# Kernel optimization log

Hardware: AMD Instinct MI355X
Metric: run time of the kernel (lower is better)

Reference implementation:

```python
import jax, jax.numpy as jnp
import numpy as np


def setup_inputs() -> dict:
    key = jax.random.key(0)
    inputs = jax.random.normal(key, (64, 4096, 256), dtype=jnp.float32)
    return {"inputs": inputs}


def reference(inputs) -> jnp.ndarray:
    # inputs: [B, N, D]; tfp.stats.covariance(sample_axis=1) -> population cov [B, D, D]
    B, N, D = inputs.shape
    mean = jnp.mean(inputs, axis=1, keepdims=True)            # [B, 1, D]
    xc = inputs - mean                                        # centered samples
    cov = jnp.einsum('bnd,bne->bde', xc, xc) / N              # [B, D, D]
    # band_part(ones, 0, -1) keeps the UPPER triangle (incl. diagonal);
    # boolean_mask flattens row-major -> triu entries in row-major order.
    iu, ju = jnp.triu_indices(D)
    return cov[:, iu, ju]                                     # [B, D*(D+1)//2]
```

## Files before the change

### kernel.cpp

```cpp
#include <hip/hip_runtime.h>
#include <hip/hip_bf16.h>
#include <stdint.h>

typedef unsigned short u16;
typedef unsigned int   u32;

#define NB   64
#define NN   4096
#define ND   256
#define NTRI 32896
#define NSPLIT 4
#define KROWS  1024
#define NCHUNK 16

__device__ __forceinline__ u32 cvtpk(float lo, float hi) {
  u32 r;
  asm("v_cvt_pk_bf16_f32 %0, %1, %2" : "=v"(r) : "v"(lo), "v"(hi));
  return r;
}
__device__ __forceinline__ float b2f_lo(u32 v) {
  union { u32 u; float f; } x; x.u = v << 16; return x.f;
}
__device__ __forceinline__ float b2f_hi(u32 v) {
  union { u32 u; float f; } x; x.u = v & 0xffff0000u; return x.f;
}

typedef __attribute__((ext_vector_type(8))) __bf16 bf16x8;
typedef __attribute__((ext_vector_type(4))) float  f32x4;

__global__ __launch_bounds__(768) void k_cov(const float* __restrict__ in,
                                             u16* __restrict__ covp,
                                             float* __restrict__ part) {
  __shared__ alignas(16) u16 Lt[2][2][256][32];
  __shared__ float msum[8][256];

  int blk = blockIdx.x;
  int b = blk >> 2, s = blk & 3;
  int t = threadIdx.x;
  int w = t >> 6, lane = t & 63;

  int tsel = w >> 2;
  int quad = w & 3;
  int wr = quad >> 1, wc = quad & 1;
  int ti = (tsel == 2) ? 1 : 0;
  int tj = (tsel == 0) ? 0 : 1;
  bool diag = (ti == tj);
  bool alive = !(diag && quad == 2);
  int fr = lane & 15, fg = lane >> 4;
  int dpA = ti * 128 + wr * 64;
  int dpB = tj * 128 + wc * 64;

  int aoffB[4], boffB[4];
  int jj = (fg ^ (fr >> 2)) << 4;
#pragma unroll
  for (int m = 0; m < 4; ++m) aoffB[m] = (dpA + m * 16 + fr) * 64 + jj;
#pragma unroll
  for (int n = 0; n < 4; ++n) boffB[n] = (dpB + n * 16 + fr) * 64 + jj;

  bool stager = (w < 8);
  int c4 = lane;
  int ksw = w >> 2;
  int xw = w & 3;
  int swz = ((xw ^ (c4 & 3)) << 4);

  f32x4 acc[4][4];
  f32x4 zero = {0.f, 0.f, 0.f, 0.f};
#pragma unroll
  for (int m = 0; m < 4; ++m)
#pragma unroll
    for (int n = 0; n < 4; ++n) acc[m][n] = zero;

  const float4* in4 = (const float4*)(in + (size_t)b * NN * ND);
  int rbase0 = (s * KROWS + w * 8) * 64 + c4;

  float4 ms = make_float4(0.f, 0.f, 0.f, 0.f);
  float4 s0, s1, s2, s3, s4, s5, s6, s7;
  uint4 q0, q1, q2, q3;

#define ISSUE(C)                                                \
  if (stager && (C) < NCHUNK) {                                 \
    int rb = rbase0 + (C) * 4096;                               \
    s0 = in4[rb + 0 * 64]; s1 = in4[rb + 1 * 64];               \
    s2 = in4[rb + 2 * 64]; s3 = in4[rb + 3 * 64];               \
    s4 = in4[rb + 4 * 64]; s5 = in4[rb + 5 * 64];               \
    s6 = in4[rb + 6 * 64]; s7 = in4[rb + 7 * 64];               \
  }

#define CVT()                                                                 \
  if (stager) {                                                               \
    ms.x += s0.x + s1.x + s2.x + s3.x + s4.x + s5.x + s6.x + s7.x;            \
    ms.y += s0.y + s1.y + s2.y + s3.y + s4.y + s5.y + s6.y + s7.y;            \
    ms.z += s0.z + s1.z + s2.z + s3.z + s4.z + s5.z + s6.z + s7.z;            \
    ms.w += s0.w + s1.w + s2.w + s3.w + s4.w + s5.w + s6.w + s7.w;            \
    q0 = make_uint4(cvtpk(s0.x, s1.x), cvtpk(s2.x, s3.x),                     \
                    cvtpk(s4.x, s5.x), cvtpk(s6.x, s7.x));                    \
    q1 = make_uint4(cvtpk(s0.y, s1.y), cvtpk(s2.y, s3.y),                     \
                    cvtpk(s4.y, s5.y), cvtpk(s6.y, s7.y));                    \
    q2 = make_uint4(cvtpk(s0.z, s1.z), cvtpk(s2.z, s3.z),                     \
                    cvtpk(s4.z, s5.z), cvtpk(s6.z, s7.z));                    \
    q3 = make_uint4(cvtpk(s0.w, s1.w), cvtpk(s2.w, s3.w),                     \
                    cvtpk(s4.w, s5.w), cvtpk(s6.w, s7.w));                    \
  }

#define WRITE(BUF)                                                            \
  if (stager) {                                                               \
    char* pl = (char*)&Lt[BUF][ksw][0][0] + swz;                              \
    *(uint4*)(pl + (c4 * 4 + 0) * 64) = q0;                                   \
    *(uint4*)(pl + (c4 * 4 + 1) * 64) = q1;                                   \
    *(uint4*)(pl + (c4 * 4 + 2) * 64) = q2;                                   \
    *(uint4*)(pl + (c4 * 4 + 3) * 64) = q3;                                   \
  }

#define COMPUTE(BUF)                                                          \
  if (alive) {                                                                \
    _Pragma("unroll")                                                         \
    for (int ks = 0; ks < 2; ++ks) {                                          \
      const char* pl = (const char*)&Lt[BUF][ks][0][0];                       \
      bf16x8 af[4], bfv[4];                                                   \
      _Pragma("unroll")                                                       \
      for (int m = 0; m < 4; ++m) af[m] = *(const bf16x8*)(pl + aoffB[m]);    \
      _Pragma("unroll")                                                       \
      for (int n = 0; n < 4; ++n) bfv[n] = *(const bf16x8*)(pl + boffB[n]);   \
      _Pragma("unroll")                                                       \
      for (int m = 0; m < 4; ++m)                                             \
        _Pragma("unroll")                                                     \
        for (int n = 0; n < 4; ++n)                                           \
          acc[m][n] = __builtin_amdgcn_mfma_f32_16x16x32_bf16(                \
              af[m], bfv[n], acc[m][n], 0, 0, 0);                             \
    }                                                                         \
  }

  ISSUE(0);
  CVT();
  ISSUE(1);
  WRITE(0);
  __syncthreads();
  for (int c = 0; c < NCHUNK - 1; ++c) {
    CVT();
    ISSUE(c + 2);
    WRITE((c + 1) & 1);
    COMPUTE(c & 1);
    __syncthreads();
  }
  COMPUTE((NCHUNK - 1) & 1);

  if (stager) *(float4*)&msum[w][c4 * 4] = ms;
  __syncthreads();
  if (t < 256) {
    float m = 0.f;
#pragma unroll
    for (int q = 0; q < 8; ++q) m += msum[q][t];
    part[(size_t)(b * 4 + s) * 256 + t] = m;
  }

  if (alive) {
    u16* cp = covp + ((size_t)(s * 192 + b * 3 + tsel) << 14);
#pragma unroll
    for (int m = 0; m < 4; ++m) {
      int liB = wr * 64 + m * 16 + fg * 4;
#pragma unroll
      for (int n = 0; n < 4; ++n) {
        int lj = wc * 64 + n * 16 + fr;
        uint2 pk;
        pk.x = cvtpk(acc[m][n][0], acc[m][n][1]);
        pk.y = cvtpk(acc[m][n][2], acc[m][n][3]);
        *(uint2*)(cp + lj * 128 + liB) = pk;
      }
    }
  }
#undef ISSUE
#undef CVT
#undef WRITE
#undef COMPUTE
}

__global__ __launch_bounds__(256) void k_fin(const u16* __restrict__ covp,
                                             const float* __restrict__ part,
                                             float* __restrict__ out) {
  __shared__ float mean_s[256];
  __shared__ float Lf[64][130];
  int blk = blockIdx.x;
  int tile = blk >> 1, half = blk & 1;
  int b = tile / 3, tsel = tile % 3;
  int ti = (tsel == 2) ? 1 : 0;
  int tj = (tsel == 0) ? 0 : 1;
  int t = threadIdx.x;

  float m = 0.f;
#pragma unroll
  for (int q = 0; q < NSPLIT; ++q) m += part[(size_t)(b * 4 + q) * 256 + t];
  mean_s[t] = m * (1.f / 4096.f);

  const u32* cp0 = (const u32*)(covp + ((size_t)(0 * 192 + tile) << 14));
  const u32* cp1 = (const u32*)(covp + ((size_t)(1 * 192 + tile) << 14));
  const u32* cp2 = (const u32*)(covp + ((size_t)(2 * 192 + tile) << 14));
  const u32* cp3 = (const u32*)(covp + ((size_t)(3 * 192 + tile) << 14));

#pragma unroll 4
  for (int k = 0; k < 16; ++k) {
    int idx  = k * 256 + t;
    int li2h = idx & 31, lj = idx >> 5;
    int e2 = lj * 64 + half * 32 + li2h;
    u32 v0 = cp0[e2], v1 = cp1[e2], v2 = cp2[e2], v3 = cp3[e2];
    Lf[li2h * 2 + 0][lj] = b2f_lo(v0) + b2f_lo(v1) + b2f_lo(v2) + b2f_lo(v3);
    Lf[li2h * 2 + 1][lj] = b2f_hi(v0) + b2f_hi(v1) + b2f_hi(v2) + b2f_hi(v3);
  }
  __syncthreads();

  const float inv = 1.f / 4096.f;
  float* ob = out + (size_t)b * NTRI;
#pragma unroll 4
  for (int e0 = 0; e0 < 8192; e0 += 256) {
    int e = e0 + t;
    int ll = e >> 7, lj = e & 127;
    int i = ti * 128 + half * 64 + ll;
    int j = tj * 128 + lj;
    if (j >= i) {
      int ro = i * 256 - ((i * (i - 1)) >> 1) - i;
      ob[ro + j] = Lf[ll][lj] * inv - mean_s[i] * mean_s[j];
    }
  }
}

__global__ __launch_bounds__(256) void k_cov_f32(const float* __restrict__ in,
                                                 float* __restrict__ out) {
  int blk = blockIdx.x;
  int b = blk / 10, ts = blk % 10;
  int ti, tj;
  if (ts < 4)      { ti = 0; tj = ts; }
  else if (ts < 7) { ti = 1; tj = ts - 3; }
  else if (ts < 9) { ti = 2; tj = ts - 5; }
  else             { ti = 3; tj = 3; }
  bool diag = (ti == tj);

  __shared__ float Pa[32][68];
  __shared__ float Pb[32][68];
  __shared__ float smA[64], smB[64];
  int t = threadIdx.x;
  if (t < 64) { smA[t] = 0.f; smB[t] = 0.f; }
  float acc[4][4] = {};
  int ri = t >> 4, rj = t & 15;
  const float* base = in + (size_t)b * NN * ND;

  for (int ks = 0; ks < 128; ++ks) {
    int nk = ks * 32;
    __syncthreads();
    for (int cc = t; cc < 512; cc += 256) {
      int r = cc >> 4, c4 = (cc & 15) << 2;
      *(float4*)&Pa[r][c4] = *(const float4*)(base + (size_t)(nk + r) * ND + ti * 64 + c4);
      if (!diag)
        *(float4*)&Pb[r][c4] = *(const float4*)(base + (size_t)(nk + r) * ND + tj * 64 + c4);
    }
    __syncthreads();
    if (t < 64) {
      float s = 0.f;
      for (int r = 0; r < 32; ++r) s += Pa[r][t];
      smA[t] += s;
    } else if (!diag && t < 128) {
      float s = 0.f;
      for (int r = 0; r < 32; ++r) s += Pb[r][t - 64];
      smB[t - 64] += s;
    }
    float(*Pbb)[68] = diag ? Pa : Pb;
    for (int k = 0; k < 32; ++k) {
      float4 a = *(const float4*)&Pa[k][ri << 2];
      float4 v = *(const float4*)&Pbb[k][rj << 2];
      float av[4] = {a.x, a.y, a.z, a.w};
      float bv[4] = {v.x, v.y, v.z, v.w};
#pragma unroll
      for (int e = 0; e < 4; ++e)
#pragma unroll
        for (int f = 0; f < 4; ++f) acc[e][f] += av[e] * bv[f];
    }
  }
  __syncthreads();
  const float inv = 1.f / 4096.f;
  const float* mB = diag ? smA : smB;
#pragma unroll
  for (int e = 0; e < 4; ++e) {
    int i = ti * 64 + (ri << 2) + e;
    float mi = smA[(ri << 2) + e] * inv;
    int ro = i * 256 - ((i * (i - 1)) >> 1) - i;
#pragma unroll
    for (int f = 0; f < 4; ++f) {
      int j = tj * 64 + (rj << 2) + f;
      if (j >= i)
        out[(size_t)b * NTRI + ro + j] = acc[e][f] * inv - mi * mB[(rj << 2) + f] * inv;
    }
  }
}

extern "C" void kernel_launch(void* const* d_in, const int* in_sizes, int n_in,
                              void* d_out, int out_size, void* d_ws, size_t ws_size,
                              hipStream_t stream) {
  const float* in = (const float*)d_in[0];
  float* out = (float*)d_out;

  const size_t COVP_B = (size_t)NSPLIT * 192 * 16384 * 2;
  const size_t PART_B = (size_t)NB * NSPLIT * 256 * 4;
  const size_t need = COVP_B + PART_B;

  if (ws_size >= need) {
    u16*   covp = (u16*)d_ws;
    float* part = (float*)((char*)d_ws + COVP_B);
    k_cov<<<NB * NSPLIT, 768, 0, stream>>>(in, covp, part);
    k_fin<<<NB * 3 * 2, 256, 0, stream>>>(covp, part, out);
  } else {
    k_cov_f32<<<NB * 10, 256, 0, stream>>>(in, out);
  }
}
```

Measured before the change: 61.17 us.

## Double the K chunk per pipeline stage and skip lower-triangle loads in finalize

Each pipeline stage now stages 16 rows per warp, giving 128 rows per chunk instead of 64. This halves the number of chunks and barriers, and each compute step runs four k-slices instead of two. Conversion and LDS write are fused into one step done before the next global load is issued, and the LDS tile doubles in size. The finalize kernel also skips loading partial covariance entries of diagonal tiles that fall below the diagonal and are never written out. In exchange, register pressure is higher (16 float4 staging registers) and occupancy may drop because of the larger shared memory footprint.

Result: slower. 65.55 us (+7.1%).

```diff
diff --git a/kernel.cpp b/kernel.cpp
--- a/kernel.cpp
+++ b/kernel.cpp
@@ -11,7 +11,7 @@
 #define NTRI 32896
 #define NSPLIT 4
 #define KROWS  1024
-#define NCHUNK 16
+#define NCHUNK 8
 
 __device__ __forceinline__ u32 cvtpk(float lo, float hi) {
   u32 r;
@@ -31,7 +31,7 @@
 __global__ __launch_bounds__(768) void k_cov(const float* __restrict__ in,
                                              u16* __restrict__ covp,
                                              float* __restrict__ part) {
-  __shared__ alignas(16) u16 Lt[2][2][256][32];
+  __shared__ alignas(16) u16 Lt[2][4][256][32];
   __shared__ float msum[8][256];
 
   int blk = blockIdx.x;
@@ -59,9 +59,8 @@
 
   bool stager = (w < 8);
   int c4 = lane;
-  int ksw = w >> 2;
-  int xw = w & 3;
-  int swz = ((xw ^ (c4 & 3)) << 4);
+  int ksw = w >> 1;
+  int xw = (w & 1) * 2;
 
   f32x4 acc[4][4];
   f32x4 zero = {0.f, 0.f, 0.f, 0.f};
@@ -71,50 +70,55 @@
     for (int n = 0; n < 4; ++n) acc[m][n] = zero;
 
   const float4* in4 = (const float4*)(in + (size_t)b * NN * ND);
-  int rbase0 = (s * KROWS + w * 8) * 64 + c4;
+  int rbase0 = (s * KROWS + w * 16) * 64 + c4;
 
   float4 ms = make_float4(0.f, 0.f, 0.f, 0.f);
   float4 s0, s1, s2, s3, s4, s5, s6, s7;
-  uint4 q0, q1, q2, q3;
-
-#define ISSUE(C)                                                \
-  if (stager && (C) < NCHUNK) {                                 \
-    int rb = rbase0 + (C) * 4096;                               \
-    s0 = in4[rb + 0 * 64]; s1 = in4[rb + 1 * 64];               \
-    s2 = in4[rb + 2 * 64]; s3 = in4[rb + 3 * 64];               \
-    s4 = in4[rb + 4 * 64]; s5 = in4[rb + 5 * 64];               \
-    s6 = in4[rb + 6 * 64]; s7 = in4[rb + 7 * 64];               \
-  }
-
-#define CVT()                                                                 \
+  float4 s8, s9, s10, s11, s12, s13, s14, s15;
+
+#define ISSUE(C)                                                   \
+  if (stager && (C) < NCHUNK) {                                    \
+    int rb = rbase0 + (C) * 8192;                                  \
+    s0  = in4[rb + 0 * 64];  s1  = in4[rb + 1 * 64];               \
+    s2  = in4[rb + 2 * 64];  s3  = in4[rb + 3 * 64];               \
+    s4  = in4[rb + 4 * 64];  s5  = in4[rb + 5 * 64];               \
+    s6  = in4[rb + 6 * 64];  s7  = in4[rb + 7 * 64];               \
+    s8  = in4[rb + 8 * 64];  s9  = in4[rb + 9 * 64];               \
+    s10 = in4[rb + 10 * 64]; s11 = in4[rb + 11 * 64];              \
+    s12 = in4[rb + 12 * 64]; s13 = in4[rb + 13 * 64];              \
+    s14 = in4[rb + 14 * 64]; s15 = in4[rb + 15 * 64];              \
+  }
+
+#define CVT_WRITE_H(BUF, H, r0, r1, r2, r3, r4, r5, r6, r7)                   \
   if (stager) {                                                               \
-    ms.x += s0.x + s1.x + s2.x + s3.x + s4.x + s5.x + s6.x + s7.x;            \
-    ms.y += s0.y + s1.y + s2.y + s3.y + s4.y + s5.y + s6.y + s7.y;            \
-    ms.z += s0.z + s1.z + s2.z + s3.z + s4.z + s5.z + s6.z + s7.z;            \
-    ms.w += s0.w + s1.w + s2.w + s3.w + s4.w + s5.w + s6.w + s7.w;            \
-    q0 = make_uint4(cvtpk(s0.x, s1.x), cvtpk(s2.x, s3.x),                     \
-                    cvtpk(s4.x, s5.x), cvtpk(s6.x, s7.x));                    \
-    q1 = make_uint4(cvtpk(s0.y, s1.y), cvtpk(s2.y, s3.y),                     \
-                    cvtpk(s4.y, s5.y), cvtpk(s6.y, s7.y));                    \
-    q2 = make_uint4(cvtpk(s0.z, s1.z), cvtpk(s2.z, s3.z),                     \
-                    cvtpk(s4.z, s5.z), cvtpk(s6.z, s7.z));                    \
-    q3 = make_uint4(cvtpk(s0.w, s1.w), cvtpk(s2.w, s3.w),                     \
-                    cvtpk(s4.w, s5.w), cvtpk(s6.w, s7.w));                    \
-  }
-
-#define WRITE(BUF)                                                            \
-  if (stager) {                                                               \
-    char* pl = (char*)&Lt[BUF][ksw][0][0] + swz;                              \
-    *(uint4*)(pl + (c4 * 4 + 0) * 64) = q0;                                   \
-    *(uint4*)(pl + (c4 * 4 + 1) * 64) = q1;                                   \
-    *(uint4*)(pl + (c4 * 4 + 2) * 64) = q2;                                   \
-    *(uint4*)(pl + (c4 * 4 + 3) * 64) = q3;                                   \
-  }
+    ms.x += r0.x + r1.x + r2.x + r3.x + r4.x + r5.x + r6.x + r7.x;            \
+    ms.y += r0.y + r1.y + r2.y + r3.y + r4.y + r5.y + r6.y + r7.y;            \
+    ms.z += r0.z + r1.z + r2.z + r3.z + r4.z + r5.z + r6.z + r7.z;            \
+    ms.w += r0.w + r1.w + r2.w + r3.w + r4.w + r5.w + r6.w + r7.w;            \
+    int ph = (((xw + (H)) ^ (c4 & 3)) << 4);                                  \
+    char* pl = (char*)&Lt[BUF][ksw][0][0] + ph;                               \
+    *(uint4*)(pl + (c4 * 4 + 0) * 64) =                                       \
+      make_uint4(cvtpk(r0.x, r1.x), cvtpk(r2.x, r3.x),                        \
+                 cvtpk(r4.x, r5.x), cvtpk(r6.x, r7.x));                       \
+    *(uint4*)(pl + (c4 * 4 + 1) * 64) =                                       \
+      make_uint4(cvtpk(r0.y, r1.y), cvtpk(r2.y, r3.y),                        \
+                 cvtpk(r4.y, r5.y), cvtpk(r6.y, r7.y));                       \
+    *(uint4*)(pl + (c4 * 4 + 2) * 64) =                                       \
+      make_uint4(cvtpk(r0.z, r1.z), cvtpk(r2.z, r3.z),                        \
+                 cvtpk(r4.z, r5.z), cvtpk(r6.z, r7.z));                       \
+    *(uint4*)(pl + (c4 * 4 + 3) * 64) =                                       \
+      make_uint4(cvtpk(r0.w, r1.w), cvtpk(r2.w, r3.w),                        \
+                 cvtpk(r4.w, r5.w), cvtpk(r6.w, r7.w));                       \
+  }
+
+#define CVT_WRITE(BUF)                                                        \
+  CVT_WRITE_H(BUF, 0, s0, s1, s2, s3, s4, s5, s6, s7);                        \
+  CVT_WRITE_H(BUF, 1, s8, s9, s10, s11, s12, s13, s14, s15);
 
 #define COMPUTE(BUF)                                                          \
   if (alive) {                                                                \
     _Pragma("unroll")                                                         \
-    for (int ks = 0; ks < 2; ++ks) {                                          \
+    for (int ks = 0; ks < 4; ++ks) {                                          \
       const char* pl = (const char*)&Lt[BUF][ks][0][0];                       \
       bf16x8 af[4], bfv[4];                                                   \
       _Pragma("unroll")                                                       \
@@ -131,14 +135,12 @@
   }
 
   ISSUE(0);
-  CVT();
+  CVT_WRITE(0);
   ISSUE(1);
-  WRITE(0);
   __syncthreads();
   for (int c = 0; c < NCHUNK - 1; ++c) {
-    CVT();
+    CVT_WRITE((c + 1) & 1);
     ISSUE(c + 2);
-    WRITE((c + 1) & 1);
     COMPUTE(c & 1);
     __syncthreads();
   }
@@ -169,8 +171,8 @@
     }
   }
 #undef ISSUE
-#undef CVT
-#undef WRITE
+#undef CVT_WRITE_H
+#undef CVT_WRITE
 #undef COMPUTE
 }
 
@@ -184,6 +186,7 @@
   int b = tile / 3, tsel = tile % 3;
   int ti = (tsel == 2) ? 1 : 0;
   int tj = (tsel == 0) ? 0 : 1;
+  bool dtile = (ti == tj);
   int t = threadIdx.x;
 
   float m = 0.f;
@@ -200,6 +203,7 @@
   for (int k = 0; k < 16; ++k) {
     int idx  = k * 256 + t;
     int li2h = idx & 31, lj = idx >> 5;
+    if (dtile && lj < half * 64 + li2h * 2) continue;
     int e2 = lj * 64 + half * 32 + li2h;
     u32 v0 = cp0[e2], v1 = cp1[e2], v2 = cp2[e2], v3 = cp3[e2];
     Lf[li2h * 2 + 0][lj] = b2f_lo(v0) + b2f_lo(v1) + b2f_lo(v2) + b2f_lo(v3);
```
